# Kernel optimization log

Measured on AMD Instinct MI355X. Metric: run time of the kernel, lower is better.

Reference implementation:

```python
import jax, jax.numpy as jnp
import numpy as np

D_HEAD = 64


def setup_inputs() -> dict:
    key = jax.random.key(0)
    ks = jax.random.split(key, 9)
    B, S, D, H, Dh = 2, 2048, 1024, 16, D_HEAD
    scale = 0.02
    return {
        "normalized_resid_pre": jax.random.normal(ks[0], (B, S, D), jnp.float32),
        "W_Q": jax.random.normal(ks[1], (H, D, Dh), jnp.float32) * scale,
        "W_K": jax.random.normal(ks[2], (H, D, Dh), jnp.float32) * scale,
        "W_V": jax.random.normal(ks[3], (H, D, Dh), jnp.float32) * scale,
        "W_O": jax.random.normal(ks[4], (H, Dh, D), jnp.float32) * scale,
        "b_Q": jax.random.normal(ks[5], (H, Dh), jnp.float32) * scale,
        "b_K": jax.random.normal(ks[6], (H, Dh), jnp.float32) * scale,
        "b_V": jax.random.normal(ks[7], (H, Dh), jnp.float32) * scale,
        "b_O": jax.random.normal(ks[8], (D,), jnp.float32) * scale,
    }


def reference(normalized_resid_pre, W_Q, W_K, W_V, W_O, b_Q, b_K, b_V, b_O):
    x = normalized_resid_pre  # [b, s, d]
    IGNORE = jnp.float32(-1e5)
    q = jnp.einsum('bsd,hde->bshe', x, W_Q) + b_Q  # [b, s, h, dh]
    k = jnp.einsum('bsd,hde->bshe', x, W_K) + b_K
    v = jnp.einsum('bsd,hde->bshe', x, W_V) + b_V
    scores = jnp.einsum('bqhe,bkhe->bhqk', q, k) / jnp.sqrt(jnp.float32(D_HEAD))
    S = scores.shape[-1]
    causal = jnp.tril(jnp.ones((S, S), dtype=bool))  # True where allowed
    scores = jnp.where(causal, scores, IGNORE)
    pattern = jax.nn.softmax(scores, axis=-1)
    z = jnp.einsum('bkhe,bhqk->bqhe', v, pattern)
    attn_out = jnp.einsum('bqhe,hed->bqd', z, W_O) + b_O
    return attn_out
```

## Files before the change

kernel.cpp:

```cpp
#include <hip/hip_runtime.h>

typedef float f32x4 __attribute__((ext_vector_type(4)));
typedef __bf16 bf16x8_t __attribute__((ext_vector_type(8)));
typedef __bf16 bf16x4_t __attribute__((ext_vector_type(4)));
typedef unsigned int u32x2 __attribute__((ext_vector_type(2)));

#define GLOAD16(gptr, lptr)                                                        \
  __builtin_amdgcn_global_load_lds((const __attribute__((address_space(1))) void*)(gptr), \
                                   (__attribute__((address_space(3))) void*)(lptr), 16, 0, 0)

__device__ inline float fexp2(float x) {
  float r;
  asm("v_exp_f32 %0, %1" : "=v"(r) : "v"(x));
  return r;
}

union VFu { bf16x8_t v8; u32x2 w[2]; };

#define TRR(d, B, OFF) \
  asm volatile("ds_read_b64_tr_b16 %0, %1 offset:" OFF : "=v"(d) : "v"(B))

__global__ __launch_bounds__(256) void k_prep(const float* __restrict__ x,
                                              const float* __restrict__ wq,
                                              const float* __restrict__ wk,
                                              const float* __restrict__ wv,
                                              const float* __restrict__ wo,
                                              const float* __restrict__ bq,
                                              const float* __restrict__ bk,
                                              const float* __restrict__ bv,
                                              __bf16* __restrict__ xb,
                                              __bf16* __restrict__ wb1,
                                              __bf16* __restrict__ wb2,
                                              float* __restrict__ b1) {
  __shared__ __bf16 tr[64][64];
  int bid = blockIdx.x, t = threadIdx.x;
  if (bid < 4096) {
    int i = bid * 256 + t;
    float4 a = reinterpret_cast<const float4*>(x)[i];
    bf16x4_t o;
    o[0] = (__bf16)a.x; o[1] = (__bf16)a.y; o[2] = (__bf16)a.z; o[3] = (__bf16)a.w;
    reinterpret_cast<bf16x4_t*>(xb)[i] = o;
  } else if (bid < 4864) {
    int k = bid - 4096;
    int dt = k & 15, h = (k >> 4) & 15, p = k >> 8;
    const float* W = (p == 0) ? wq : (p == 1) ? wk : wv;
#pragma unroll
    for (int i = 0; i < 4; ++i) {
      int fl = i * 1024 + t * 4;
      int dd = fl >> 6, e = fl & 63;
      float4 a = *reinterpret_cast<const float4*>(W + ((size_t)(h * 1024 + dt * 64 + dd) * 64 + e));
      tr[e + 0][dd] = (__bf16)a.x; tr[e + 1][dd] = (__bf16)a.y;
      tr[e + 2][dd] = (__bf16)a.z; tr[e + 3][dd] = (__bf16)a.w;
    }
    __syncthreads();
#pragma unroll
    for (int i = 0; i < 2; ++i) {
      int ch = i * 256 + t;
      int e = ch >> 3, c8 = ch & 7;
      *reinterpret_cast<bf16x8_t*>(wb1 + ((size_t)(p * 1024 + h * 64 + e) * 1024 + dt * 64 + c8 * 8)) =
          *reinterpret_cast<const bf16x8_t*>(&tr[e][c8 * 8]);
    }
  } else if (bid < 5120) {
    int k = bid - 4864;
    int nt = k & 15, h = k >> 4;
#pragma unroll
    for (int i = 0; i < 4; ++i) {
      int fl = i * 1024 + t * 4;
      int e = fl >> 6, nn = fl & 63;
      float4 a = *reinterpret_cast<const float4*>(wo + ((size_t)(h * 64 + e) * 1024 + nt * 64 + nn));
      tr[nn + 0][e] = (__bf16)a.x; tr[nn + 1][e] = (__bf16)a.y;
      tr[nn + 2][e] = (__bf16)a.z; tr[nn + 3][e] = (__bf16)a.w;
    }
    __syncthreads();
#pragma unroll
    for (int i = 0; i < 2; ++i) {
      int ch = i * 256 + t;
      int nn = ch >> 3, c8 = ch & 7;
      *reinterpret_cast<bf16x8_t*>(wb2 + ((size_t)(nt * 64 + nn) * 1024 + h * 64 + c8 * 8)) =
          *reinterpret_cast<const bf16x8_t*>(&tr[nn][c8 * 8]);
    }
  } else {
    int n = (bid - 5120) * 256 + t;
    if (n < 3072) {
      int p = n >> 10, he = n & 1023;
      const float* s = (p == 0) ? bq : (p == 1) ? bk : bv;
      b1[n] = s[he];
    }
  }
}

template <typename OutT, int MODE, int NT>
__global__ __launch_bounds__(256) void k_gemm(const __bf16* __restrict__ A,
                                              const __bf16* __restrict__ Bt,
                                              const float* __restrict__ bias,
                                              OutT* __restrict__ C, int N, int K) {
  __shared__ __bf16 As[128 * 64];
  __shared__ __bf16 Bs[NT * 64];
  constexpr int NR = NT / 32;
  constexpr int BI = NT / 32;
  int t = threadIdx.x, l = t & 63;
  int lo = l & 15, hi = l >> 4;
  int w = t >> 6;
  int m0 = blockIdx.y * 128, n0 = blockIdx.x * NT;
  int wm = (w >> 1) * 64, wn = (w & 1) * (NT / 2);
  f32x4 acc[4][NR] = {};
  for (int k0 = 0; k0 < K; k0 += 64) {
    __syncthreads();
#pragma unroll
    for (int it = 0; it < 4; ++it) {
      int idx = it * 256 + t;
      int row = idx >> 3, c = idx & 7;
      int cs = (c ^ (row & 7)) * 8;
      GLOAD16(A + (size_t)(m0 + row) * K + k0 + cs, (char*)As + (it * 256 + (t & ~63)) * 16);
    }
#pragma unroll
    for (int it = 0; it < BI; ++it) {
      int idx = it * 256 + t;
      int row = idx >> 3, c = idx & 7;
      int cs = (c ^ (row & 7)) * 8;
      GLOAD16(Bt + (size_t)(n0 + row) * K + k0 + cs, (char*)Bs + (it * 256 + (t & ~63)) * 16);
    }
    __syncthreads();
#pragma unroll
    for (int kc = 0; kc < 2; ++kc) {
      bf16x8_t af[4], bfr[NR];
#pragma unroll
      for (int mi = 0; mi < 4; ++mi) {
        int row = wm + mi * 16 + lo;
        af[mi] = *reinterpret_cast<const bf16x8_t*>(
            (char*)As + row * 128 + (((kc * 4 + hi) ^ (row & 7)) << 4));
      }
#pragma unroll
      for (int ni = 0; ni < NR; ++ni) {
        int row = wn + ni * 16 + lo;
        bfr[ni] = *reinterpret_cast<const bf16x8_t*>(
            (char*)Bs + row * 128 + (((kc * 4 + hi) ^ (row & 7)) << 4));
      }
#pragma unroll
      for (int mi = 0; mi < 4; ++mi)
#pragma unroll
        for (int ni = 0; ni < NR; ++ni)
          acc[mi][ni] = __builtin_amdgcn_mfma_f32_16x16x32_bf16(af[mi], bfr[ni], acc[mi][ni], 0, 0, 0);
    }
  }
  float qs = (MODE == 1 && blockIdx.x * NT < 1024) ? 0.18033688f : 1.0f;
#pragma unroll
  for (int ni = 0; ni < NR; ++ni) {
    int n = n0 + wn + ni * 16 + lo;
    float bv = bias[n];
    int p = n >> 10, hh = (n >> 6) & 15, e = n & 63;
#pragma unroll
    for (int mi = 0; mi < 4; ++mi) {
#pragma unroll
      for (int r = 0; r < 4; ++r) {
        int m = m0 + wm + mi * 16 + hi * 4 + r;
        if (MODE == 0) {
          C[(size_t)m * N + n] = (OutT)(acc[mi][ni][r] + bv);
        } else {
          int b = m >> 11, sr = m & 2047;
          C[(size_t)(p * 32 + b * 16 + hh) * 131072 + sr * 64 + e] =
              (OutT)((acc[mi][ni][r] + bv) * qs);
        }
      }
    }
  }
}

__global__ __launch_bounds__(256, 4) void k_attn(const __bf16* __restrict__ QKVh,
                                                 __bf16* __restrict__ Z) {
  __shared__ __bf16 Ks[2][64 * 64];
  __shared__ __bf16 Vs[2][64 * 64];
  __shared__ __bf16 Ps[64 * 64];
  int t = threadIdx.x, l = t & 63, w = t >> 6;
  int lo = l & 15, hi = l >> 4;
  int bid = blockIdx.x;
  int xcd = bid & 7, kk = bid >> 3;
  int qi = kk & 31, bhl = kk >> 5;
  int bh = xcd * 4 + bhl;
  int b = bh >> 4, h = bh & 15;
  int wg = w >> 1, wl = w & 1;
  int j = wg ? qi : 63 - qi;
  int qbase = j * 32 + wl * 16;
  int ntH = ((63 - qi) >> 1) + 1;
  int ntW = (j >> 1) + 1;

  const __bf16* Qbase = QKVh + (size_t)bh * 131072;
  const __bf16* Kbase = QKVh + (size_t)(32 + bh) * 131072;
  const __bf16* Vbase = QKVh + (size_t)(64 + bh) * 131072;

  int kSrc[2], vSrc[2];
#pragma unroll
  for (int it = 0; it < 2; ++it) {
    int idx = it * 256 + t;
    int row = idx >> 3, c = idx & 7;
    kSrc[it] = row * 64 + ((c ^ (row & 7)) * 8);
    int kv = ((idx >> 1) & 3) | (((idx >> 5) & 1) << 2) | (((idx >> 3) & 3) << 3) |
             (((idx >> 8) & 1) << 5);
    int e0s = ((idx & 1) << 3) | (((idx >> 6) & 3) << 4);
    vSrc[it] = kv * 64 + e0s;
  }

  bf16x8_t qf[2];
  {
    const __bf16* qptr = Qbase + (qbase + lo) * 64;
    qf[0] = *reinterpret_cast<const bf16x8_t*>(qptr + hi * 8);
    qf[1] = *reinterpret_cast<const bf16x8_t*>(qptr + 32 + hi * 8);
  }

  f32x4 zacc[4] = {};
  float lsum = 0.f;
  float mrow = -1e30f;

#define STAGE_KV(buf, tile)                                                             \
  {                                                                                     \
    GLOAD16(Kbase + (tile) * 4096 + kSrc[0], (char*)Ks[buf] + (t & ~63) * 16);          \
    GLOAD16(Kbase + (tile) * 4096 + kSrc[1], (char*)Ks[buf] + 4096 + (t & ~63) * 16);   \
    GLOAD16(Vbase + (tile) * 4096 + vSrc[0], (char*)Vs[buf] + (t & ~63) * 16);          \
    GLOAD16(Vbase + (tile) * 4096 + vSrc[1], (char*)Vs[buf] + 4096 + (t & ~63) * 16);   \
  }

  STAGE_KV(0, 0);
  __syncthreads();

  for (int tile = 0; tile < ntH; ++tile) {
    int cur = tile & 1, kv0 = tile * 64;
    bool havenext = (tile + 1 < ntH);
    if (havenext) {
      STAGE_KV(cur ^ 1, tile + 1);
      __builtin_amdgcn_sched_barrier(0);
    }
    if (tile < ntW) {
      f32x4 s[4] = {};
      __builtin_amdgcn_s_setprio(1);
#pragma unroll
      for (int cb = 0; cb < 4; ++cb) {
        int krow = cb * 16 + lo;
        const char* kp = (const char*)Ks[cur] + krow * 128;
        bf16x8_t kf0 = *reinterpret_cast<const bf16x8_t*>(kp + ((hi ^ (krow & 7)) << 4));
        bf16x8_t kf1 = *reinterpret_cast<const bf16x8_t*>(kp + (((4 + hi) ^ (krow & 7)) << 4));
        s[cb] = __builtin_amdgcn_mfma_f32_16x16x32_bf16(kf0, qf[0], s[cb], 0, 0, 0);
        s[cb] = __builtin_amdgcn_mfma_f32_16x16x32_bf16(kf1, qf[1], s[cb], 0, 0, 0);
      }
      __builtin_amdgcn_s_setprio(0);
      {
        int qabs = qbase + lo;
        bool msk = (tile == ntW - 1);
        float mt = -1e30f;
#pragma unroll
        for (int cb = 0; cb < 4; ++cb)
#pragma unroll
          for (int r = 0; r < 4; ++r) {
            float v = s[cb][r];
            if (msk && (kv0 + cb * 16 + hi * 4 + r > qabs)) v = -1e30f;
            s[cb][r] = v;
            mt = fmaxf(mt, v);
          }
        mt = fmaxf(mt, __shfl_xor(mt, 16));
        mt = fmaxf(mt, __shfl_xor(mt, 32));
        if (!__all(mt - mrow <= 8.0f)) {
          float mnew = fmaxf(mrow, mt);
          float alpha = fexp2(mrow - mnew);
          mrow = mnew;
          lsum *= alpha;
#pragma unroll
          for (int r = 0; r < 4; ++r) {
            float at = __shfl(alpha, hi * 4 + r);
#pragma unroll
            for (int e0 = 0; e0 < 4; ++e0) zacc[e0][r] *= at;
          }
        }
        float psum = 0.f;
        int prow = w * 16 + lo;
        char* prp = (char*)Ps + prow * 128 + (hi & 1) * 8;
        int rsw = prow & 7;
#pragma unroll
        for (int cb = 0; cb < 4; ++cb) {
          bf16x4_t pp;
#pragma unroll
          for (int r = 0; r < 4; ++r) {
            float p = fexp2(s[cb][r] - mrow);
            psum += p;
            pp[r] = (__bf16)p;
          }
          *reinterpret_cast<bf16x4_t*>(prp + (((cb * 2 + (hi >> 1)) ^ rsw) << 4)) = pp;
        }
        lsum += psum;
      }
      __builtin_amdgcn_s_setprio(1);
      {
        const __attribute__((address_space(3))) char* vb =
            (const __attribute__((address_space(3))) char*)((char*)Vs[cur]) + l * 8;
        int arow = w * 16 + lo;
        {
          bf16x8_t pf = *reinterpret_cast<const bf16x8_t*>(
              (char*)Ps + arow * 128 + (((hi) ^ (arow & 7)) << 4));
          VFu u0, u1, u2, u3;
          TRR(u0.w[0], vb, "0");    TRR(u0.w[1], vb, "512");
          TRR(u1.w[0], vb, "1024"); TRR(u1.w[1], vb, "1536");
          TRR(u2.w[0], vb, "2048"); TRR(u2.w[1], vb, "2560");
          TRR(u3.w[0], vb, "3072"); TRR(u3.w[1], vb, "3584");
          asm volatile("s_waitcnt lgkmcnt(0)" ::: "memory");
          __builtin_amdgcn_sched_barrier(0);
          zacc[0] = __builtin_amdgcn_mfma_f32_16x16x32_bf16(pf, u0.v8, zacc[0], 0, 0, 0);
          zacc[1] = __builtin_amdgcn_mfma_f32_16x16x32_bf16(pf, u1.v8, zacc[1], 0, 0, 0);
          zacc[2] = __builtin_amdgcn_mfma_f32_16x16x32_bf16(pf, u2.v8, zacc[2], 0, 0, 0);
          zacc[3] = __builtin_amdgcn_mfma_f32_16x16x32_bf16(pf, u3.v8, zacc[3], 0, 0, 0);
        }
        {
          bf16x8_t pf = *reinterpret_cast<const bf16x8_t*>(
              (char*)Ps + arow * 128 + (((4 + hi) ^ (arow & 7)) << 4));
          VFu u0, u1, u2, u3;
          TRR(u0.w[0], vb, "4096"); TRR(u0.w[1], vb, "4608");
          TRR(u1.w[0], vb, "5120"); TRR(u1.w[1], vb, "5632");
          TRR(u2.w[0], vb, "6144"); TRR(u2.w[1], vb, "6656");
          TRR(u3.w[0], vb, "7168"); TRR(u3.w[1], vb, "7680");
          asm volatile("s_waitcnt lgkmcnt(0)" ::: "memory");
          __builtin_amdgcn_sched_barrier(0);
          zacc[0] = __builtin_amdgcn_mfma_f32_16x16x32_bf16(pf, u0.v8, zacc[0], 0, 0, 0);
          zacc[1] = __builtin_amdgcn_mfma_f32_16x16x32_bf16(pf, u1.v8, zacc[1], 0, 0, 0);
          zacc[2] = __builtin_amdgcn_mfma_f32_16x16x32_bf16(pf, u2.v8, zacc[2], 0, 0, 0);
          zacc[3] = __builtin_amdgcn_mfma_f32_16x16x32_bf16(pf, u3.v8, zacc[3], 0, 0, 0);
        }
      }
      __builtin_amdgcn_s_setprio(0);
    }
    __syncthreads();
  }

  float lt = lsum;
  lt += __shfl_xor(lt, 16);
  lt += __shfl_xor(lt, 32);
  float inv = 1.0f / lt;
#pragma unroll
  for (int r = 0; r < 4; ++r) {
    float lv = __shfl(inv, hi * 4 + r);
    size_t row = (size_t)(b * 2048 + qbase + hi * 4 + r);
#pragma unroll
    for (int e0 = 0; e0 < 4; ++e0)
      Z[row * 1024 + h * 64 + e0 * 16 + lo] = (__bf16)(zacc[e0][r] * lv);
  }
#undef STAGE_KV
}


extern "C" void kernel_launch(void* const* d_in, const int* in_sizes, int n_in,
                              void* d_out, int out_size, void* d_ws, size_t ws_size,
                              hipStream_t stream) {
  const float* x  = (const float*)d_in[0];
  const float* wq = (const float*)d_in[1];
  const float* wk = (const float*)d_in[2];
  const float* wv = (const float*)d_in[3];
  const float* wo = (const float*)d_in[4];
  const float* bq = (const float*)d_in[5];
  const float* bk = (const float*)d_in[6];
  const float* bv = (const float*)d_in[7];
  const float* bo = (const float*)d_in[8];
  float* out = (float*)d_out;

  char* ws = (char*)d_ws;
  __bf16* Xb   = (__bf16*)(ws);
  __bf16* WB1  = (__bf16*)(ws + 8388608);
  float*  B1   = (float*)(ws + 14680064);
  __bf16* WB2  = (__bf16*)(ws + 14692352);
  __bf16* QKVh = (__bf16*)(ws + 16789504);
  __bf16* Zb   = Xb;

  k_prep<<<5132, 256, 0, stream>>>(x, wq, wk, wv, wo, bq, bk, bv, Xb, WB1, WB2, B1);
  k_gemm<__bf16, 1, 128><<<dim3(24, 32), 256, 0, stream>>>(Xb, WB1, B1, QKVh, 3072, 1024);
  k_attn<<<1024, 256, 0, stream>>>(QKVh, Zb);
  k_gemm<float, 0, 64><<<dim3(16, 32), 256, 0, stream>>>(Zb, WB2, bo, out, 1024, 1024);
}
```

Before: 124.9 us.

## Remap GEMM blocks per XCD and rebalance causal attention query tiles per wave

```diff
diff --git a/kernel.cpp b/kernel.cpp
--- a/kernel.cpp
+++ b/kernel.cpp
@@ -101,7 +101,12 @@
   int t = threadIdx.x, l = t & 63;
   int lo = l & 15, hi = l >> 4;
   int w = t >> 6;
-  int m0 = blockIdx.y * 128, n0 = blockIdx.x * NT;
+  int bid = blockIdx.x;
+  int xcd = bid & 7, loc = bid >> 3;
+  int xc = N / NT;
+  int yy = loc / xc;
+  int xx = loc - yy * xc;
+  int m0 = (xcd * 4 + yy) * 128, n0 = xx * NT;
   int wm = (w >> 1) * 64, wn = (w & 1) * (NT / 2);
   f32x4 acc[4][NR] = {};
   for (int k0 = 0; k0 < K; k0 += 64) {
@@ -143,7 +148,7 @@
           acc[mi][ni] = __builtin_amdgcn_mfma_f32_16x16x32_bf16(af[mi], bfr[ni], acc[mi][ni], 0, 0, 0);
     }
   }
-  float qs = (MODE == 1 && blockIdx.x * NT < 1024) ? 0.18033688f : 1.0f;
+  float qs = (MODE == 1 && n0 < 1024) ? 0.18033688f : 1.0f;
 #pragma unroll
   for (int ni = 0; ni < NR; ++ni) {
     int n = n0 + wn + ni * 16 + lo;
@@ -175,14 +180,13 @@
   int lo = l & 15, hi = l >> 4;
   int bid = blockIdx.x;
   int xcd = bid & 7, kk = bid >> 3;
-  int qi = kk & 31, bhl = kk >> 5;
+  int i = kk & 31, bhl = kk >> 5;
   int bh = xcd * 4 + bhl;
   int b = bh >> 4, h = bh & 15;
-  int wg = w >> 1, wl = w & 1;
-  int j = wg ? qi : 63 - qi;
-  int qbase = j * 32 + wl * 16;
-  int ntH = ((63 - qi) >> 1) + 1;
-  int ntW = (j >> 1) + 1;
+  int s16 = (w >> 1) * 64 + ((w & 1) ? (63 - i) : i);
+  int qbase = s16 * 16;
+  int ntW = (s16 >> 2) + 1;
+  int ntH = ((127 - i) >> 2) + 1;
 
   const __bf16* Qbase = QKVh + (size_t)bh * 131072;
   const __bf16* Kbase = QKVh + (size_t)(32 + bh) * 131072;
@@ -244,17 +248,20 @@
       __builtin_amdgcn_s_setprio(0);
       {
         int qabs = qbase + lo;
-        bool msk = (tile == ntW - 1);
+        if (tile == ntW - 1) {
+#pragma unroll
+          for (int cb = 0; cb < 4; ++cb)
+#pragma unroll
+            for (int r = 0; r < 4; ++r)
+              if (kv0 + cb * 16 + hi * 4 + r > qabs) s[cb][r] = -1e30f;
+        }
         float mt = -1e30f;
 #pragma unroll
-        for (int cb = 0; cb < 4; ++cb)
-#pragma unroll
-          for (int r = 0; r < 4; ++r) {
-            float v = s[cb][r];
-            if (msk && (kv0 + cb * 16 + hi * 4 + r > qabs)) v = -1e30f;
-            s[cb][r] = v;
-            mt = fmaxf(mt, v);
-          }
+        for (int cb = 0; cb < 4; ++cb) {
+          float m01 = fmaxf(s[cb][0], s[cb][1]);
+          float m23 = fmaxf(s[cb][2], s[cb][3]);
+          mt = fmaxf(mt, fmaxf(m01, m23));
+        }
         mt = fmaxf(mt, __shfl_xor(mt, 16));
         mt = fmaxf(mt, __shfl_xor(mt, 32));
         if (!__all(mt - mrow <= 8.0f)) {
@@ -366,7 +373,7 @@
   __bf16* Zb   = Xb;
 
   k_prep<<<5132, 256, 0, stream>>>(x, wq, wk, wv, wo, bq, bk, bv, Xb, WB1, WB2, B1);
-  k_gemm<__bf16, 1, 128><<<dim3(24, 32), 256, 0, stream>>>(Xb, WB1, B1, QKVh, 3072, 1024);
+  k_gemm<__bf16, 1, 128><<<768, 256, 0, stream>>>(Xb, WB1, B1, QKVh, 3072, 1024);
   k_attn<<<1024, 256, 0, stream>>>(QKVh, Zb);
-  k_gemm<float, 0, 64><<<dim3(16, 32), 256, 0, stream>>>(Zb, WB2, bo, out, 1024, 1024);
-}
+  k_gemm<float, 0, 64><<<512, 256, 0, stream>>>(Zb, WB2, bo, out, 1024, 1024);
+}
```

New measurement: 122.2 us. 1.02x faster.
